# Performance work log

Measured on AMD Instinct MI355X. Metric: run time of the kernel, lower is better.

The kernel has to match this reference:

```python
import jax, jax.numpy as jnp
import numpy as np

B = 32768

def setup_inputs() -> dict:
    key = jax.random.key(0)
    ks = jax.random.split(key, 6)
    x = jax.random.normal(ks[0], (B, 1, 28, 28), dtype=jnp.float32)
    conv_w = jax.random.normal(ks[1], (4, 1, 2, 2), dtype=jnp.float32) * 0.5   # Conv2d(1,4,2,2) OIHW
    conv_b = jax.random.normal(ks[2], (4,), dtype=jnp.float32) * 0.1
    q_w = jax.random.normal(ks[3], (4, 4), dtype=jnp.float32) * 0.5            # Linear(4,4,bias=False), (out,in)
    lin_w = jax.random.normal(ks[4], (10, 1568), dtype=jnp.float32) * 0.02     # Linear(1568,10), (out,in)
    lin_b = jax.random.normal(ks[5], (10,), dtype=jnp.float32) * 0.02
    return {"x": x, "conv_w": conv_w, "conv_b": conv_b, "q_w": q_w, "lin_w": lin_w, "lin_b": lin_b}

def reference(x, conv_w, conv_b, q_w, lin_w, lin_b):
    b = x.shape[0]
    # conv branch: (B,1,28,28) -> (B,4,14,14)
    conv = jax.lax.conv_general_dilated(
        x, conv_w, window_strides=(2, 2), padding='VALID',
        dimension_numbers=('NCHW', 'OIHW', 'NCHW')) + conv_b[None, :, None, None]
    cls_feat = conv.reshape(b, -1)  # (B,784)
    # quantum branch: all 196 non-overlapping 2x2 patches in loop (r,c) order,
    # each flattened row-major to 4 values, then one batched 4x4 linear.
    img = x.reshape(b, 28, 28)
    patches = img.reshape(b, 14, 2, 14, 2).transpose(0, 1, 3, 2, 4).reshape(b, 196, 4)
    qfeat = jnp.einsum('bpi,oi->bpo', patches, q_w).reshape(b, 196 * 4)  # (B,784)
    combined = jnp.concatenate([cls_feat, qfeat], axis=1)  # (B,1568)
    logits = combined @ lin_w.T + lin_b
    return jax.nn.log_softmax(logits, axis=-1)
```

## Files before the change

### kernel.cpp

```cpp
#include <hip/hip_runtime.h>
#include <math.h>

#define NOUT   10
#define ROWLEN 784
#define WTOT   (NOUT*ROWLEN)

__global__ __launch_bounds__(256)
void quanv_prep(const float* __restrict__ conv_w,
                const float* __restrict__ conv_b,
                const float* __restrict__ q_w,
                const float* __restrict__ lin_w,
                const float* __restrict__ lin_b,
                float* __restrict__ W)
{
    const int t = threadIdx.x;

    for (int idx = blockIdx.x * 256 + t; idx < WTOT; idx += gridDim.x * 256) {
        const int o = idx / ROWLEN;
        const int j = idx - o * ROWLEN;
        const int h = j / 28, w = j - h * 28;
        const int p = (h >> 1) * 14 + (w >> 1);
        const int k = (h & 1) * 2 + (w & 1);
        float s = 0.f;
        #pragma unroll
        for (int c = 0; c < 4; ++c)
            s += conv_w[c * 4 + k] * lin_w[o * 1568 + c * 196 + p];
        #pragma unroll
        for (int q = 0; q < 4; ++q)
            s += q_w[q * 4 + k] * lin_w[o * 1568 + 784 + p * 4 + q];
        W[idx] = s;
    }

    if (blockIdx.x == 0) {
        __shared__ float rs[40];
        const int lane = t & 7;
        for (int pair = t >> 3; pair < 40; pair += 32) {
            const int o = pair >> 2, c = pair & 3;
            const float* base = lin_w + o * 1568 + c * 196;
            float s = 0.f;
            #pragma unroll
            for (int p = 0; p < 196; p += 8) {
                const int pp = p + lane;
                if (pp < 196) s += base[pp];
            }
            s += __shfl_xor(s, 1);
            s += __shfl_xor(s, 2);
            s += __shfl_xor(s, 4);
            if (lane == 0) rs[pair] = s;
        }
        __syncthreads();
        if (t < NOUT) {
            float s = lin_b[t];
            #pragma unroll
            for (int c = 0; c < 4; ++c) s += conv_b[c] * rs[t * 4 + c];
            W[WTOT + t] = s;
        }
    }
}

__global__ __launch_bounds__(256, 4)
void quanv_main(const float* __restrict__ x,
                const float* __restrict__ Wg,
                float* __restrict__ out)
{
    __shared__ float Wl[WTOT];
    __shared__ float bias[NOUT];

    const int t     = threadIdx.x;
    const int lane  = t & 63;
    const int wv    = t >> 6;
    const int l     = lane & 15;
    const int grp   = lane >> 4;
    const int pair  = grp >> 1;
    const int gp    = grp & 1;
    const int obase = gp * 5;
    const int r0    = blockIdx.x * 32 + wv * 8 + pair * 4;

    const float* __restrict__ xr = x + (size_t)r0 * ROWLEN;

    float4 px0[4], px1[4];
    #pragma unroll
    for (int r = 0; r < 4; ++r) {
        px0[r] = *(const float4*)(xr + r * ROWLEN + 4 * l);
        px1[r] = *(const float4*)(xr + r * ROWLEN + 4 * l + 64);
    }

    {
        const float4* __restrict__ src = (const float4*)Wg;
        float4* dst = (float4*)Wl;
        #pragma unroll
        for (int i = 0; i < 8; ++i) {
            const int idx = t + 256 * i;
            if (idx < WTOT / 4) dst[idx] = src[idx];
        }
        if (t < NOUT) bias[t] = Wg[WTOT + t];
    }
    __syncthreads();

    float acc[4][5];
    #pragma unroll
    for (int r = 0; r < 4; ++r)
        #pragma unroll
        for (int o = 0; o < 5; ++o) acc[r][o] = 0.f;

    const int wb = obase * ROWLEN;

    #pragma unroll
    for (int i = 0; i < 12; ++i) {
        float4 cur[4];
        #pragma unroll
        for (int r = 0; r < 4; ++r) cur[r] = ((i & 1) == 0) ? px0[r] : px1[r];

        const int ni = i + 2;
        if (ni < 12) {
            const int nfo = 4 * l + 64 * ni;
            #pragma unroll
            for (int r = 0; r < 4; ++r) {
                const float4 v = *(const float4*)(xr + r * ROWLEN + nfo);
                if ((i & 1) == 0) px0[r] = v; else px1[r] = v;
            }
        } else if (ni == 12) {
            const int tfo = 768 + 4 * (l & 3);
            #pragma unroll
            for (int r = 0; r < 4; ++r)
                px0[r] = *(const float4*)(xr + r * ROWLEN + tfo);
        }

        const int fo = 4 * l + 64 * i;
        #pragma unroll
        for (int o = 0; o < 5; ++o) {
            const float4 w4 = *(const float4*)&Wl[wb + o * ROWLEN + fo];
            #pragma unroll
            for (int r = 0; r < 4; ++r)
                acc[r][o] = fmaf(cur[r].x, w4.x, fmaf(cur[r].y, w4.y,
                            fmaf(cur[r].z, w4.z, fmaf(cur[r].w, w4.w, acc[r][o]))));
        }
    }
    if (l < 4) {
        const int fo = 768 + 4 * l;
        #pragma unroll
        for (int o = 0; o < 5; ++o) {
            const float4 w4 = *(const float4*)&Wl[wb + o * ROWLEN + fo];
            #pragma unroll
            for (int r = 0; r < 4; ++r)
                acc[r][o] = fmaf(px0[r].x, w4.x, fmaf(px0[r].y, w4.y,
                            fmaf(px0[r].z, w4.z, fmaf(px0[r].w, w4.w, acc[r][o]))));
        }
    }

    #pragma unroll
    for (int r = 0; r < 4; ++r)
        #pragma unroll
        for (int o = 0; o < 5; ++o) {
            acc[r][o] += __shfl_xor(acc[r][o], 1);
            acc[r][o] += __shfl_xor(acc[r][o], 2);
            acc[r][o] += __shfl_xor(acc[r][o], 4);
            acc[r][o] += __shfl_xor(acc[r][o], 8);
        }

    float own[4][5], part[4][5];
    #pragma unroll
    for (int r = 0; r < 4; ++r)
        #pragma unroll
        for (int o = 0; o < 5; ++o) {
            own[r][o]  = acc[r][o] + bias[obase + o];
            part[r][o] = __shfl_xor(own[r][o], 16);
        }

    float lgA[10], lgB[10];
    #pragma unroll
    for (int o = 0; o < 5; ++o) {
        lgA[o]     = gp ? part[2][o] : own[0][o];
        lgA[o + 5] = gp ? own[2][o]  : part[0][o];
        lgB[o]     = gp ? part[3][o] : own[1][o];
        lgB[o + 5] = gp ? own[3][o]  : part[1][o];
    }

    float mA = -1e30f, mB = -1e30f;
    #pragma unroll
    for (int o = 0; o < 10; ++o) { mA = fmaxf(mA, lgA[o]); mB = fmaxf(mB, lgB[o]); }
    float sA = 0.f, sB = 0.f;
    #pragma unroll
    for (int o = 0; o < 10; ++o) { sA += expf(lgA[o] - mA); sB += expf(lgB[o] - mB); }
    const float lseA = mA + logf(sA);
    const float lseB = mB + logf(sB);

    if (l < NOUT) {
        float vA = lgA[0], vB = lgB[0];
        #pragma unroll
        for (int o = 1; o < 10; ++o) {
            vA = (l == o) ? lgA[o] : vA;
            vB = (l == o) ? lgB[o] : vB;
        }
        const int rA = r0 + 2 * gp;
        out[(size_t)rA * NOUT + l]       = vA - lseA;
        out[(size_t)(rA + 1) * NOUT + l] = vB - lseB;
    }
}

extern "C" void kernel_launch(void* const* d_in, const int* in_sizes, int n_in,
                              void* d_out, int out_size, void* d_ws, size_t ws_size,
                              hipStream_t stream) {
    const float* x      = (const float*)d_in[0];
    const float* conv_w = (const float*)d_in[1];
    const float* conv_b = (const float*)d_in[2];
    const float* q_w    = (const float*)d_in[3];
    const float* lin_w  = (const float*)d_in[4];
    const float* lin_b  = (const float*)d_in[5];
    float* out = (float*)d_out;
    float* W   = (float*)d_ws;

    const int rows = in_sizes[0] / ROWLEN;

    quanv_prep<<<31, 256, 0, stream>>>(conv_w, conv_b, q_w, lin_w, lin_b, W);
    quanv_main<<<rows / 32, 256, 0, stream>>>(x, W, out);
}
```

Before: 31.90 us.

## Use 1024-thread blocks with split-K halves per wave for 64 rows per block

Each block now has 1024 threads and handles 64 rows. Each wave covers 4 rows and splits the 784-element reduction into two halves (kh), so the per-lane loop length drops from 12 to 6 iterations. A cross-half shuffle (xor 32) combines the partial sums, and the log-softmax is reorganized so each lane group produces one row. This halves how often the 31KB weight matrix is staged into LDS per row and shortens the dependency chain per thread. In exchange, each block is larger, and launch_bounds(1024,8) may constrain registers.

```diff
diff --git a/kernel.cpp b/kernel.cpp
--- a/kernel.cpp
+++ b/kernel.cpp
@@ -58,7 +58,7 @@
     }
 }
 
-__global__ __launch_bounds__(256, 4)
+__global__ __launch_bounds__(1024, 8)
 void quanv_main(const float* __restrict__ x,
                 const float* __restrict__ Wg,
                 float* __restrict__ out)
@@ -66,17 +66,16 @@
     __shared__ float Wl[WTOT];
     __shared__ float bias[NOUT];
 
-    const int t     = threadIdx.x;
-    const int lane  = t & 63;
-    const int wv    = t >> 6;
-    const int l     = lane & 15;
-    const int grp   = lane >> 4;
-    const int pair  = grp >> 1;
-    const int gp    = grp & 1;
-    const int obase = gp * 5;
-    const int r0    = blockIdx.x * 32 + wv * 8 + pair * 4;
-
-    const float* __restrict__ xr = x + (size_t)r0 * ROWLEN;
+    const int t    = threadIdx.x;
+    const int lane = t & 63;
+    const int wv   = t >> 6;
+    const int l    = lane & 15;
+    const int g2   = lane >> 4;
+    const int oh   = g2 & 1;
+    const int kh   = g2 >> 1;
+    const int r0   = blockIdx.x * 64 + wv * 4;
+
+    const float* __restrict__ xr = x + (size_t)r0 * ROWLEN + kh * 392;
 
     float4 px0[4], px1[4];
     #pragma unroll
@@ -89,8 +88,8 @@
         const float4* __restrict__ src = (const float4*)Wg;
         float4* dst = (float4*)Wl;
         #pragma unroll
-        for (int i = 0; i < 8; ++i) {
-            const int idx = t + 256 * i;
+        for (int i = 0; i < 2; ++i) {
+            const int idx = t + 1024 * i;
             if (idx < WTOT / 4) dst[idx] = src[idx];
         }
         if (t < NOUT) bias[t] = Wg[WTOT + t];
@@ -103,24 +102,24 @@
         #pragma unroll
         for (int o = 0; o < 5; ++o) acc[r][o] = 0.f;
 
-    const int wb = obase * ROWLEN;
-
-    #pragma unroll
-    for (int i = 0; i < 12; ++i) {
+    const int wb = oh * 5 * ROWLEN + kh * 392;
+
+    #pragma unroll
+    for (int i = 0; i < 6; ++i) {
         float4 cur[4];
         #pragma unroll
         for (int r = 0; r < 4; ++r) cur[r] = ((i & 1) == 0) ? px0[r] : px1[r];
 
         const int ni = i + 2;
-        if (ni < 12) {
+        if (ni < 6) {
             const int nfo = 4 * l + 64 * ni;
             #pragma unroll
             for (int r = 0; r < 4; ++r) {
                 const float4 v = *(const float4*)(xr + r * ROWLEN + nfo);
                 if ((i & 1) == 0) px0[r] = v; else px1[r] = v;
             }
-        } else if (ni == 12) {
-            const int tfo = 768 + 4 * (l & 3);
+        } else if (ni == 6) {
+            const int tfo = 384 + 4 * (l & 1);
             #pragma unroll
             for (int r = 0; r < 4; ++r)
                 px0[r] = *(const float4*)(xr + r * ROWLEN + tfo);
@@ -136,8 +135,8 @@
                             fmaf(cur[r].z, w4.z, fmaf(cur[r].w, w4.w, acc[r][o]))));
         }
     }
-    if (l < 4) {
-        const int fo = 768 + 4 * l;
+    if (l < 2) {
+        const int fo = 384 + 4 * l;
         #pragma unroll
         for (int o = 0; o < 5; ++o) {
             const float4 w4 = *(const float4*)&Wl[wb + o * ROWLEN + fo];
@@ -156,45 +155,46 @@
             acc[r][o] += __shfl_xor(acc[r][o], 2);
             acc[r][o] += __shfl_xor(acc[r][o], 4);
             acc[r][o] += __shfl_xor(acc[r][o], 8);
-        }
-
-    float own[4][5], part[4][5];
+            acc[r][o] += __shfl_xor(acc[r][o], 32);
+        }
+
+    float own[4][5], ex[4][5];
     #pragma unroll
     for (int r = 0; r < 4; ++r)
         #pragma unroll
         for (int o = 0; o < 5; ++o) {
-            own[r][o]  = acc[r][o] + bias[obase + o];
-            part[r][o] = __shfl_xor(own[r][o], 16);
-        }
-
-    float lgA[10], lgB[10];
+            own[r][o] = acc[r][o] + bias[oh * 5 + o];
+            ex[r][o]  = __shfl_xor(own[r][o], 16);
+        }
+
+    float lg[NOUT];
     #pragma unroll
     for (int o = 0; o < 5; ++o) {
-        lgA[o]     = gp ? part[2][o] : own[0][o];
-        lgA[o + 5] = gp ? own[2][o]  : part[0][o];
-        lgB[o]     = gp ? part[3][o] : own[1][o];
-        lgB[o + 5] = gp ? own[3][o]  : part[1][o];
-    }
-
-    float mA = -1e30f, mB = -1e30f;
-    #pragma unroll
-    for (int o = 0; o < 10; ++o) { mA = fmaxf(mA, lgA[o]); mB = fmaxf(mB, lgB[o]); }
-    float sA = 0.f, sB = 0.f;
-    #pragma unroll
-    for (int o = 0; o < 10; ++o) { sA += expf(lgA[o] - mA); sB += expf(lgB[o] - mB); }
-    const float lseA = mA + logf(sA);
-    const float lseB = mB + logf(sB);
+        float osel = own[0][o];
+        osel = (g2 == 1) ? own[1][o] : osel;
+        osel = (g2 == 2) ? own[2][o] : osel;
+        osel = (g2 == 3) ? own[3][o] : osel;
+        float esel = ex[0][o];
+        esel = (g2 == 1) ? ex[1][o] : esel;
+        esel = (g2 == 2) ? ex[2][o] : esel;
+        esel = (g2 == 3) ? ex[3][o] : esel;
+        lg[o]     = oh ? esel : osel;
+        lg[o + 5] = oh ? osel : esel;
+    }
+
+    float m = -1e30f;
+    #pragma unroll
+    for (int o = 0; o < NOUT; ++o) m = fmaxf(m, lg[o]);
+    float s = 0.f;
+    #pragma unroll
+    for (int o = 0; o < NOUT; ++o) s += expf(lg[o] - m);
+    const float lse = m + logf(s);
 
     if (l < NOUT) {
-        float vA = lgA[0], vB = lgB[0];
-        #pragma unroll
-        for (int o = 1; o < 10; ++o) {
-            vA = (l == o) ? lgA[o] : vA;
-            vB = (l == o) ? lgB[o] : vB;
-        }
-        const int rA = r0 + 2 * gp;
-        out[(size_t)rA * NOUT + l]       = vA - lseA;
-        out[(size_t)(rA + 1) * NOUT + l] = vB - lseB;
+        float v = lg[0];
+        #pragma unroll
+        for (int o = 1; o < NOUT; ++o) v = (l == o) ? lg[o] : v;
+        out[(size_t)(r0 + g2) * NOUT + l] = v - lse;
     }
 }
 
@@ -213,5 +213,5 @@
     const int rows = in_sizes[0] / ROWLEN;
 
     quanv_prep<<<31, 256, 0, stream>>>(conv_w, conv_b, q_w, lin_w, lin_b, W);
-    quanv_main<<<rows / 32, 256, 0, stream>>>(x, W, out);
+    quanv_main<<<rows / 64, 1024, 0, stream>>>(x, W, out);
 }
```

Result: slower. 113.4 us (+255.6%).
